# Kernel optimization log

Measured on AMD Instinct MI355X. Metric: run time of the kernel, lower is better.

Reference implementation:

```python
import jax, jax.numpy as jnp
import numpy as np

B, SQ, SK, D = 4, 2048, 2048, 1024


def setup_inputs() -> dict:
    key = jax.random.key(0)
    ks = jax.random.split(key, 8)
    s = 1.0 / np.sqrt(D)
    return {
        "input_seq": jax.random.normal(ks[0], (B, SQ, D), jnp.float32),
        "condition_seq": jax.random.normal(ks[1], (B, SK, D), jnp.float32),
        "Wq": jax.random.normal(ks[2], (D, D), jnp.float32) * s,
        "bq": jnp.zeros((D,), jnp.float32),
        "Wk": jax.random.normal(ks[3], (D, D), jnp.float32) * s,
        "bk": jnp.zeros((D,), jnp.float32),
        "Wv": jax.random.normal(ks[4], (D, D), jnp.float32) * s,
        "bv": jnp.zeros((D,), jnp.float32),
    }


def reference(input_seq, condition_seq, Wq, bq, Wk, bk, Wv, bv):
    # Linear projections (torch Linear: x @ W.T + b)
    q = jnp.einsum("bsd,ed->bse", input_seq, Wq) + bq        # [B,SQ,D]
    k = jnp.einsum("btd,ed->bte", condition_seq, Wk) + bk    # [B,SK,D]
    v = jnp.einsum("btd,ed->bte", condition_seq, Wv) + bv    # [B,SK,D]
    # NOTE: original module omits the 1/sqrt(d) scaling — kept faithful.
    scores = jnp.einsum("bse,bte->bst", q, k)                # [B,SQ,SK]
    attn = jax.nn.softmax(scores, axis=-1)
    attended = jnp.einsum("bst,bte->bse", attn, v)           # [B,SQ,D]
    return attended
```

## Files before the change

### kernel.cpp

```cpp
#include <hip/hip_runtime.h>

using f32x4  = __attribute__((ext_vector_type(4))) float;
using bf16x8 = __attribute__((ext_vector_type(8))) __bf16;
using f16x8  = __attribute__((ext_vector_type(8))) _Float16;
using u16x4  = __attribute__((ext_vector_type(4))) unsigned short;
using u16x8  = __attribute__((ext_vector_type(8))) unsigned short;

constexpr int Bb = 4, SQn = 2048, SKn = 2048, Dd = 1024;

__device__ __forceinline__ unsigned fbitsu(float x){ union{float f;unsigned u;}c; c.f=x; return c.u; }
__device__ __forceinline__ float ubitsf(unsigned u){ union{unsigned u;float f;}c; c.u=u; return c.f; }
__device__ __forceinline__ unsigned short hi_trunc(float x){ return (unsigned short)(fbitsu(x)>>16); }
__device__ __forceinline__ unsigned short hi_rne(float x){ unsigned u=fbitsu(x); return (unsigned short)((u + 0x7FFFu + ((u>>16)&1u))>>16); }
__device__ __forceinline__ float from_hi(unsigned short h){ return ubitsf(((unsigned)h)<<16); }
__device__ __forceinline__ unsigned short h_rne(float x){ _Float16 h = (_Float16)x; return __builtin_bit_cast(unsigned short, h); }
__device__ __forceinline__ float h2f(unsigned short u){ return (float)__builtin_bit_cast(_Float16, u); }

template<int DT> __device__ __forceinline__ unsigned short cvt_rne(float x){ return DT ? h_rne(x) : hi_rne(x); }
template<int DT> __device__ __forceinline__ float cvt_f(unsigned short u){ return DT ? h2f(u) : from_hi(u); }

__device__ __forceinline__ f32x4 mfma_bf16(bf16x8 a, bf16x8 b, f32x4 c){
    return __builtin_amdgcn_mfma_f32_16x16x32_bf16(a, b, c, 0, 0, 0);
}
__device__ __forceinline__ f32x4 mfma_f16(u16x8 a, u16x8 b, f32x4 c){
    return __builtin_amdgcn_mfma_f32_16x16x32_f16(
        __builtin_bit_cast(f16x8, a), __builtin_bit_cast(f16x8, b), c, 0, 0, 0);
}
template<int DT>
__device__ __forceinline__ f32x4 mfma_u16(u16x8 a, u16x8 b, f32x4 c){
    if constexpr (DT) return mfma_f16(a, b, c);
    else return __builtin_amdgcn_mfma_f32_16x16x32_bf16(
        __builtin_bit_cast(bf16x8, a), __builtin_bit_cast(bf16x8, b), c, 0, 0, 0);
}

__device__ __forceinline__ void gload16(const void* g, void* l){
    __builtin_amdgcn_global_load_lds(
        (const __attribute__((address_space(1))) unsigned int*)g,
        (__attribute__((address_space(3))) unsigned int*)l, 16, 0, 0);
}

__device__ __forceinline__ void xcd_swz(int& bx, int& by){
    const int nx = gridDim.x, nwg = nx * gridDim.y;
    int l = by * nx + bx;
    l = (l & 7) * (nwg >> 3) + (l >> 3);
    bx = l % nx; by = l / nx;
}

__global__ __launch_bounds__(256)
void split2(const float* __restrict__ x, const float* __restrict__ c,
            unsigned short* __restrict__ xh, unsigned short* __restrict__ xl,
            unsigned short* __restrict__ ch, unsigned short* __restrict__ cl,
            int n4)
{
    const int stride = gridDim.x * 256;
    for (int i = blockIdx.x * 256 + threadIdx.x; i < 2 * n4; i += stride) {
        const bool second = (i >= n4);
        const int j = second ? i - n4 : i;
        const float* in = second ? c : x;
        unsigned short* hi = second ? ch : xh;
        unsigned short* lo = second ? cl : xl;
        float a[4]; *(float4*)a = *(const float4*)(in + (size_t)j * 4);
        u16x4 h, l;
#pragma unroll
        for (int r = 0; r < 4; ++r) {
            h[r] = h_rne(a[r]);
            l[r] = h_rne(a[r] - h2f(h[r]));
        }
        *(u16x4*)&hi[(size_t)j * 4] = h;
        *(u16x4*)&lo[(size_t)j * 4] = l;
    }
}

__global__ __launch_bounds__(256)
void cvtW(const float* __restrict__ Wq, const float* __restrict__ Wk,
          const float* __restrict__ Wv,
          unsigned short* __restrict__ oq, unsigned short* __restrict__ ok,
          unsigned short* __restrict__ ov, int n4)
{
    const int stride = gridDim.x * 256;
    for (int i = blockIdx.x * 256 + threadIdx.x; i < 3 * n4; i += stride) {
        const float* src; unsigned short* dst; int j = i;
        if (j < n4)          { src = Wq; dst = oq; }
        else if (j < 2*n4)   { src = Wk; dst = ok; j -= n4; }
        else                 { src = Wv; dst = ov; j -= 2*n4; }
        float a[4]; *(float4*)a = *(const float4*)(src + (size_t)j * 4);
        u16x4 h;
#pragma unroll
        for (int r = 0; r < 4; ++r) h[r] = h_rne(a[r]);
        *(u16x4*)&dst[(size_t)j * 4] = h;
    }
}

template<int TERMS, int BM_, int BN_, int BK_, int EPI, int DT>
__global__ __launch_bounds__(256, 2)
void gemm_tile(const unsigned short* __restrict__ Ahg, const unsigned short* __restrict__ Alg,
               const unsigned short* __restrict__ Bhg, const unsigned short* __restrict__ Blg,
               const float* __restrict__ bias,
               void* __restrict__ O0v, void* __restrict__ O1v,
               int M, int N, int K, long aBS, long bBS, long oBS)
{
    constexpr int ROWB = BK_ * 2;
    constexpr int RPC  = 1024 / ROWB;
    constexpr int CA   = BM_ / RPC;
    constexpr int CB   = BN_ / RPC;
    constexpr int AI   = BM_ / 32;
    constexpr int BJ   = BN_ / 32;
    constexpr int KH   = BK_ / 32;
    static_assert(CA % 4 == 0 && CB % 4 == 0, "chunks divisible by 4 waves");

    __shared__ __align__(16) unsigned short Ash[BM_*BK_], Bsh[BN_*BK_];
    __shared__ __align__(16) unsigned short Asl[TERMS>=2?BM_*BK_:8];
    __shared__ __align__(16) unsigned short Bsl[TERMS==3?BN_*BK_:8];

    const int z = blockIdx.z;
    Ahg += (size_t)z * aBS;
    Bhg += (size_t)z * bBS;
    if (TERMS >= 2) Alg += (size_t)z * aBS;
    if (TERMS == 3) Blg += (size_t)z * bBS;

    int bx = blockIdx.x, by = blockIdx.y;
    xcd_swz(bx, by);

    const int tid = threadIdx.x, lane = tid & 63, w = tid >> 6;
    const int wr = (w >> 1) * (BM_/2), wc = (w & 1) * (BN_/2);
    const int lr = lane & 15, lg = lane >> 4;
    const int m0 = by * BM_, n0 = bx * BN_;
    constexpr int rsh = (ROWB == 64) ? 2 : 3;
    const int rowc = lane >> rsh;
    const int colb = (lane & ((1 << rsh) - 1)) << 4;
    const size_t rsBy = (size_t)K * 2;

    f32x4 acc[AI][BJ] = {};

    for (int k0 = 0; k0 < K; k0 += BK_) {
#pragma unroll
        for (int c4 = 0; c4 < CA/4; ++c4) {
            const int c = c4*4 + w;
            const size_t go = (size_t)(m0 + c*RPC + rowc) * rsBy + (size_t)k0*2 + colb;
            gload16((const char*)Ahg + go, (char*)Ash + c*1024);
            if (TERMS >= 2) gload16((const char*)Alg + go, (char*)Asl + c*1024);
        }
#pragma unroll
        for (int c4 = 0; c4 < CB/4; ++c4) {
            const int c = c4*4 + w;
            const size_t go = (size_t)(n0 + c*RPC + rowc) * rsBy + (size_t)k0*2 + colb;
            gload16((const char*)Bhg + go, (char*)Bsh + c*1024);
            if (TERMS == 3) gload16((const char*)Blg + go, (char*)Bsl + c*1024);
        }
        __syncthreads();

#pragma unroll
        for (int kk = 0; kk < KH; ++kk) {
            u16x8 ah[AI], bh[BJ];
#pragma unroll
            for (int i = 0; i < AI; ++i) ah[i] = *(const u16x8*)&Ash[(wr + i*16 + lr)*BK_ + kk*32 + lg*8];
#pragma unroll
            for (int j = 0; j < BJ; ++j) bh[j] = *(const u16x8*)&Bsh[(wc + j*16 + lr)*BK_ + kk*32 + lg*8];
            if (TERMS == 3) {
                u16x8 al[AI], bl[BJ];
#pragma unroll
                for (int i = 0; i < AI; ++i) al[i] = *(const u16x8*)&Asl[(wr + i*16 + lr)*BK_ + kk*32 + lg*8];
#pragma unroll
                for (int j = 0; j < BJ; ++j) bl[j] = *(const u16x8*)&Bsl[(wc + j*16 + lr)*BK_ + kk*32 + lg*8];
#pragma unroll
                for (int i = 0; i < AI; ++i)
#pragma unroll
                    for (int j = 0; j < BJ; ++j) {
                        acc[i][j] = mfma_u16<DT>(ah[i], bh[j], acc[i][j]);
                        acc[i][j] = mfma_u16<DT>(ah[i], bl[j], acc[i][j]);
                        acc[i][j] = mfma_u16<DT>(al[i], bh[j], acc[i][j]);
                    }
            } else if (TERMS == 2) {
                u16x8 al[AI];
#pragma unroll
                for (int i = 0; i < AI; ++i) al[i] = *(const u16x8*)&Asl[(wr + i*16 + lr)*BK_ + kk*32 + lg*8];
#pragma unroll
                for (int i = 0; i < AI; ++i)
#pragma unroll
                    for (int j = 0; j < BJ; ++j) {
                        acc[i][j] = mfma_u16<DT>(ah[i], bh[j], acc[i][j]);
                        acc[i][j] = mfma_u16<DT>(al[i], bh[j], acc[i][j]);
                    }
            } else {
#pragma unroll
                for (int i = 0; i < AI; ++i)
#pragma unroll
                    for (int j = 0; j < BJ; ++j)
                        acc[i][j] = mfma_u16<DT>(ah[i], bh[j], acc[i][j]);
            }
        }
        __syncthreads();
    }

    if (EPI == 0) {
        float* C = (float*)O0v + (size_t)z * oBS;
#pragma unroll
        for (int j = 0; j < BJ; ++j) {
            const int col = n0 + wc + j*16 + lr;
#pragma unroll
            for (int i = 0; i < AI; ++i)
#pragma unroll
                for (int r = 0; r < 4; ++r)
                    C[(size_t)(m0 + wr + i*16 + lg*4 + r) * N + col] = acc[i][j][r];
        }
    } else {
        unsigned short* Chi = (unsigned short*)O0v + (size_t)z * oBS;
        unsigned short* Clo = (unsigned short*)O1v + (size_t)z * oBS;
#pragma unroll
        for (int j = 0; j < BJ; ++j) {
            const int col = n0 + wc + j*16 + lr;
            const float bc = (EPI == 2) ? bias[col] : 0.f;
#pragma unroll
            for (int i = 0; i < AI; ++i)
#pragma unroll
                for (int r = 0; r < 4; ++r) {
                    const size_t idx = (size_t)(m0 + wr + i*16 + lg*4 + r) * N + col;
                    const float v = acc[i][j][r] + bc;
                    const unsigned short h = cvt_rne<DT>(v);
                    Chi[idx] = h;
                    Clo[idx] = cvt_rne<DT>(v - cvt_f<DT>(h));
                }
        }
    }
}

__global__ __launch_bounds__(256, 2)
void gemm_kv(const unsigned short* __restrict__ Ahg, const unsigned short* __restrict__ Alg,
             const unsigned short* __restrict__ Wk16, const unsigned short* __restrict__ Wv16,
             const float* __restrict__ bk, const float* __restrict__ bv,
             unsigned short* __restrict__ Kh, unsigned short* __restrict__ Vt,
             int M, int N, int K)
{
    constexpr int BM_ = 128, BN_ = 128, BK_ = 32;
    __shared__ __align__(16) unsigned short Ash[BM_*BK_], Asl[BM_*BK_];
    __shared__ __align__(16) unsigned short Bks[BN_*BK_], Bvs[BN_*BK_];

    int bx = blockIdx.x, by = blockIdx.y;
    xcd_swz(bx, by);

    const int tid = threadIdx.x, lane = tid & 63, w = tid >> 6;
    const int wr = (w >> 1) * 64, wc = (w & 1) * 64;
    const int lr = lane & 15, lg = lane >> 4;
    const int m0 = by * BM_, n0 = bx * BN_;
    const int rowc = lane >> 2;
    const int colb = (lane & 3) << 4;
    const size_t rsBy = (size_t)K * 2;

    f32x4 acck[4][4] = {}, accv[4][4] = {};

    for (int k0 = 0; k0 < K; k0 += BK_) {
#pragma unroll
        for (int c4 = 0; c4 < 2; ++c4) {
            const int c = c4*4 + w;
            const size_t goA = (size_t)(m0 + c*16 + rowc) * rsBy + (size_t)k0*2 + colb;
            gload16((const char*)Ahg + goA, (char*)Ash + c*1024);
            gload16((const char*)Alg + goA, (char*)Asl + c*1024);
            const size_t goB = (size_t)(n0 + c*16 + rowc) * rsBy + (size_t)k0*2 + colb;
            gload16((const char*)Wk16 + goB, (char*)Bks + c*1024);
            gload16((const char*)Wv16 + goB, (char*)Bvs + c*1024);
        }
        __syncthreads();

        u16x8 ah[4], al[4], bf[4];
#pragma unroll
        for (int i = 0; i < 4; ++i) {
            ah[i] = *(const u16x8*)&Ash[(wr + i*16 + lr)*BK_ + lg*8];
            al[i] = *(const u16x8*)&Asl[(wr + i*16 + lr)*BK_ + lg*8];
        }
#pragma unroll
        for (int j = 0; j < 4; ++j) bf[j] = *(const u16x8*)&Bks[(wc + j*16 + lr)*BK_ + lg*8];
#pragma unroll
        for (int i = 0; i < 4; ++i)
#pragma unroll
            for (int j = 0; j < 4; ++j) {
                acck[i][j] = mfma_f16(ah[i], bf[j], acck[i][j]);
                acck[i][j] = mfma_f16(al[i], bf[j], acck[i][j]);
            }
#pragma unroll
        for (int j = 0; j < 4; ++j) bf[j] = *(const u16x8*)&Bvs[(wc + j*16 + lr)*BK_ + lg*8];
#pragma unroll
        for (int i = 0; i < 4; ++i)
#pragma unroll
            for (int j = 0; j < 4; ++j) {
                accv[i][j] = mfma_f16(ah[i], bf[j], accv[i][j]);
                accv[i][j] = mfma_f16(al[i], bf[j], accv[i][j]);
            }
        __syncthreads();
    }

#pragma unroll
    for (int j = 0; j < 4; ++j) {
        const int col = n0 + wc + j*16 + lr;
        const float bck = bk[col], bcv = bv[col];
#pragma unroll
        for (int i = 0; i < 4; ++i) {
            const int row0 = m0 + wr + i*16 + lg*4;
#pragma unroll
            for (int r = 0; r < 4; ++r)
                Kh[(size_t)(row0 + r)*N + col] = h_rne(acck[i][j][r] + bck);
            const int b = row0 >> 11, t0 = row0 & 2047;
            u16x4 pk;
#pragma unroll
            for (int r = 0; r < 4; ++r) pk[r] = h_rne(accv[i][j][r] + bcv);
            *(u16x4*)&Vt[(((size_t)b*Dd + col) << 11) + t0] = pk;
        }
    }
}

template<int TERMS, int EPI>
__global__ __launch_bounds__(256, 2)
void gemm_proj(const float* __restrict__ A, const float* __restrict__ Bm,
               const float* __restrict__ bias,
               unsigned short* __restrict__ O0, unsigned short* __restrict__ O1,
               int M, int N, int K)
{
    constexpr int BM_ = 128, BN_ = 64, BK_ = 32;
    __shared__ __align__(16) unsigned short Ash[BM_*BK_], Bsh[BN_*BK_];
    __shared__ __align__(16) unsigned short Asl[TERMS==3?BM_*BK_:8], Bsl[TERMS==3?BN_*BK_:8];

    const int tid = threadIdx.x, lane = tid & 63, w = tid >> 6;
    const int wr = (w >> 1) * 64, wc = (w & 1) * 32;
    const int lr = lane & 15, lg = lane >> 4;
    const int m0 = blockIdx.y * BM_, n0 = blockIdx.x * BN_;

    f32x4 acc[4][2] = {};

    for (int k0 = 0; k0 < K; k0 += BK_) {
        float4 av[4], bv[2];
#pragma unroll
        for (int u = 0; u < 4; ++u) {
            const int f = u*256 + tid;
            av[u] = *(const float4*)(A + (size_t)(m0 + (f >> 3))*K + k0 + ((f & 7) << 2));
        }
#pragma unroll
        for (int u = 0; u < 2; ++u) {
            const int f = u*256 + tid;
            bv[u] = *(const float4*)(Bm + (size_t)(n0 + (f >> 3))*K + k0 + ((f & 7) << 2));
        }
        __syncthreads();
#pragma unroll
        for (int u = 0; u < 4; ++u) {
            const int f = u*256 + tid;
            const int row = f >> 3, ko = (f & 7) << 2;
            float a4[4]; *(float4*)a4 = av[u];
            u16x4 ah;
            if (TERMS == 3) {
                u16x4 al;
#pragma unroll
                for (int j = 0; j < 4; ++j) { ah[j] = hi_trunc(a4[j]); al[j] = hi_trunc(a4[j] - from_hi(ah[j])); }
                *(u16x4*)&Asl[row*BK_ + ko] = al;
            } else {
#pragma unroll
                for (int j = 0; j < 4; ++j) ah[j] = hi_rne(a4[j]);
            }
            *(u16x4*)&Ash[row*BK_ + ko] = ah;
        }
#pragma unroll
        for (int u = 0; u < 2; ++u) {
            const int f = u*256 + tid;
            const int row = f >> 3, ko = (f & 7) << 2;
            float b4[4]; *(float4*)b4 = bv[u];
            u16x4 bh;
            if (TERMS == 3) {
                u16x4 bl;
#pragma unroll
                for (int j = 0; j < 4; ++j) { bh[j] = hi_trunc(b4[j]); bl[j] = hi_trunc(b4[j] - from_hi(bh[j])); }
                *(u16x4*)&Bsl[row*BK_ + ko] = bl;
            } else {
#pragma unroll
                for (int j = 0; j < 4; ++j) bh[j] = hi_rne(b4[j]);
            }
            *(u16x4*)&Bsh[row*BK_ + ko] = bh;
        }
        __syncthreads();

        bf16x8 ah[4], bh[2];
#pragma unroll
        for (int i = 0; i < 4; ++i) ah[i] = *(const bf16x8*)&Ash[(wr + i*16 + lr)*BK_ + lg*8];
#pragma unroll
        for (int j = 0; j < 2; ++j) bh[j] = *(const bf16x8*)&Bsh[(wc + j*16 + lr)*BK_ + lg*8];
        if (TERMS == 3) {
            bf16x8 al[4], bl[2];
#pragma unroll
            for (int i = 0; i < 4; ++i) al[i] = *(const bf16x8*)&Asl[(wr + i*16 + lr)*BK_ + lg*8];
#pragma unroll
            for (int j = 0; j < 2; ++j) bl[j] = *(const bf16x8*)&Bsl[(wc + j*16 + lr)*BK_ + lg*8];
#pragma unroll
            for (int i = 0; i < 4; ++i)
#pragma unroll
                for (int j = 0; j < 2; ++j) {
                    acc[i][j] = mfma_bf16(ah[i], bh[j], acc[i][j]);
                    acc[i][j] = mfma_bf16(ah[i], bl[j], acc[i][j]);
                    acc[i][j] = mfma_bf16(al[i], bh[j], acc[i][j]);
                }
        } else {
#pragma unroll
            for (int i = 0; i < 4; ++i)
#pragma unroll
                for (int j = 0; j < 2; ++j)
                    acc[i][j] = mfma_bf16(ah[i], bh[j], acc[i][j]);
        }
        __syncthreads();
    }

#pragma unroll
    for (int j = 0; j < 2; ++j) {
        const int col = n0 + wc + j*16 + lr;
        const float bc = bias[col];
#pragma unroll
        for (int i = 0; i < 4; ++i) {
            if (EPI == 0) {
#pragma unroll
                for (int r = 0; r < 4; ++r) {
                    const int row = m0 + wr + i*16 + lg*4 + r;
                    const float v = acc[i][j][r] + bc;
                    const unsigned short h = h_rne(v);
                    O0[(size_t)row*N + col] = h;
                    O1[(size_t)row*N + col] = h_rne(v - h2f(h));
                }
            } else if (EPI == 2) {
#pragma unroll
                for (int r = 0; r < 4; ++r) {
                    const int row = m0 + wr + i*16 + lg*4 + r;
                    O0[(size_t)row*N + col] = h_rne(acc[i][j][r] + bc);
                }
            } else {
                const int row0 = m0 + wr + i*16 + lg*4;
                const int b = row0 >> 11, t0 = row0 & 2047;
                u16x4 pk;
#pragma unroll
                for (int r = 0; r < 4; ++r) pk[r] = h_rne(acc[i][j][r] + bc);
                *(u16x4*)&O0[(((size_t)b*Dd + col) << 11) + t0] = pk;
            }
        }
    }
}

__global__ __launch_bounds__(256)
void softmax_sp(unsigned short* __restrict__ Shi, const unsigned short* __restrict__ Slo)
{
    const int tid = threadIdx.x;
    unsigned short* ph = Shi + (size_t)blockIdx.x * SKn;
    const unsigned short* pl = Slo + (size_t)blockIdx.x * SKn;
    __shared__ float red[8];

    u16x4 h0 = *(const u16x4*)&ph[tid*4];
    u16x4 h1 = *(const u16x4*)&ph[1024 + tid*4];
    u16x4 l0 = *(const u16x4*)&pl[tid*4];
    u16x4 l1 = *(const u16x4*)&pl[1024 + tid*4];
    float v[8];
#pragma unroll
    for (int r = 0; r < 4; ++r) {
        v[r]   = h2f(h0[r]) + h2f(l0[r]);
        v[4+r] = h2f(h1[r]) + h2f(l1[r]);
    }
    float m = v[0];
#pragma unroll
    for (int r = 1; r < 8; ++r) m = fmaxf(m, v[r]);
#pragma unroll
    for (int o2 = 32; o2 > 0; o2 >>= 1) m = fmaxf(m, __shfl_down(m, o2));
    if ((tid & 63) == 0) red[tid >> 6] = m;
    __syncthreads();
    m = fmaxf(fmaxf(red[0],red[1]), fmaxf(red[2],red[3]));

    float e[8], s = 0.f;
#pragma unroll
    for (int r = 0; r < 8; ++r) { e[r] = __expf(v[r] - m); s += e[r]; }
#pragma unroll
    for (int o2 = 32; o2 > 0; o2 >>= 1) s += __shfl_down(s, o2);
    if ((tid & 63) == 0) red[4 + (tid >> 6)] = s;
    __syncthreads();
    const float inv = 1.f / ((red[4]+red[5])+(red[6]+red[7]));

    u16x4 p0, p1;
#pragma unroll
    for (int r = 0; r < 4; ++r) { p0[r] = h_rne(e[r]*inv); p1[r] = h_rne(e[4+r]*inv); }
    *(u16x4*)&ph[tid*4] = p0;
    *(u16x4*)&ph[1024 + tid*4] = p1;
}

extern "C" void kernel_launch(void* const* d_in, const int* in_sizes, int n_in,
                              void* d_out, int out_size, void* d_ws, size_t ws_size,
                              hipStream_t stream)
{
    const float* x  = (const float*)d_in[0];
    const float* c  = (const float*)d_in[1];
    const float* Wq = (const float*)d_in[2];
    const float* bq = (const float*)d_in[3];
    const float* Wk = (const float*)d_in[4];
    const float* bk = (const float*)d_in[5];
    const float* Wv = (const float*)d_in[6];
    const float* bv = (const float*)d_in[7];
    float* out = (float*)d_out;

    const size_t nQ = (size_t)Bb * SQn * Dd;
    const size_t sE = (size_t)SQn * SKn;
    const size_t nW = (size_t)Dd * Dd;
    unsigned short* Qh = (unsigned short*)d_ws;
    unsigned short* Ql = Qh + nQ;
    unsigned short* Kh = Ql + nQ;
    unsigned short* Kl = Kh + nQ;
    unsigned short* Vt = Kl + nQ;
    unsigned short* Shi = Vt + nQ;
    unsigned short* Slo = Shi + (size_t)Bb * sE;

    unsigned short* Wq16 = Kl;
    unsigned short* Wk16 = Kl + nW;
    unsigned short* Wv16 = Kl + 2*nW;

    unsigned short* xh = Shi;
    unsigned short* xl = Shi + nQ;
    unsigned short* ch = Slo;
    unsigned short* cl = Slo + nQ;

    const size_t needB = (size_t)(Shi - Qh) * 2 + (size_t)Bb * sE * 2 * 2;
    const bool batched = ws_size >= needB;

    const dim3 blk(256);

    if (batched) {
        split2<<<dim3(4096), blk, 0, stream>>>(x, c, xh, xl, ch, cl, (int)(nQ/4));
        cvtW<<<dim3(1024), blk, 0, stream>>>(Wq, Wk, Wv, Wq16, Wk16, Wv16, (int)(nW/4));

        gemm_tile<2,128,128,32,2,1><<<dim3(Dd/128, (Bb*SQn)/128), blk, 0, stream>>>(
            xh, xl, Wq16, nullptr, bq, Qh, Ql, Bb*SQn, Dd, Dd, 0, 0, 0);
        gemm_kv<<<dim3(Dd/128, (Bb*SKn)/128), blk, 0, stream>>>(
            ch, cl, Wk16, Wv16, bk, bv, Kh, Vt, Bb*SKn, Dd, Dd);

        gemm_tile<2,128,128,32,1,1><<<dim3(SKn/128, SQn/128, Bb), blk, 0, stream>>>(
            Qh, Ql, Kh, nullptr, nullptr, Shi, Slo, SQn, SKn, Dd,
            (long)SQn*Dd, (long)SKn*Dd, (long)sE);
        softmax_sp<<<dim3(Bb*SQn), blk, 0, stream>>>(Shi, Slo);
        gemm_tile<1,128,128,32,0,1><<<dim3(Dd/128, SQn/128, Bb), blk, 0, stream>>>(
            Shi, nullptr, Vt, nullptr, nullptr, out, nullptr, SQn, Dd, SKn,
            (long)sE, (long)Dd*SKn, (long)SQn*Dd);
    } else {
        unsigned short* ShiF = Shi;
        unsigned short* SloF = Shi + sE;
        gemm_proj<3,0><<<dim3(Dd/64, (Bb*SQn)/128), blk, 0, stream>>>(x, Wq, bq, Qh, Ql, Bb*SQn, Dd, Dd);
        gemm_proj<3,2><<<dim3(Dd/64, (Bb*SKn)/128), blk, 0, stream>>>(c, Wk, bk, Kh, nullptr, Bb*SKn, Dd, Dd);
        gemm_proj<1,1><<<dim3(Dd/64, (Bb*SKn)/128), blk, 0, stream>>>(c, Wv, bv, Vt, nullptr, Bb*SKn, Dd, Dd);
        for (int b = 0; b < Bb; ++b) {
            const size_t qoff = (size_t)b * SQn * Dd;
            const size_t koff = (size_t)b * SKn * Dd;
            gemm_tile<2,128,64,32,1,1><<<dim3(SKn/64, SQn/128, 1), blk, 0, stream>>>(
                Qh+qoff, Ql+qoff, Kh+koff, nullptr, nullptr, ShiF, SloF, SQn, SKn, Dd, 0, 0, 0);
            softmax_sp<<<dim3(SQn), blk, 0, stream>>>(ShiF, SloF);
            gemm_tile<1,64,64,32,0,1><<<dim3(Dd/64, SQn/64, 1), blk, 0, stream>>>(
                ShiF, nullptr, Vt+(size_t)b*Dd*SKn, nullptr, nullptr, out+qoff, nullptr,
                SQn, Dd, SKn, 0, 0, 0);
        }
    }
}
```

Before: 287.2 us.

## Double-buffer LDS tiles in projection GEMMs to overlap global loads with MFMA

Both the generic GEMM tile kernel and the fused K/V projection kernel now use two LDS buffers. The next K-slice is prefetched with direct-to-LDS loads while MFMAs run on the current one, and a partial vmcnt wait plus raw s_barrier replaces __syncthreads. This targets the load-latency stalls that serialized each K iteration. It doubles LDS use, which may reduce occupancy under launch_bounds(256,2), and it relies on the LPT count matching the exact number of outstanding loads per thread.

```diff
diff --git a/kernel.cpp b/kernel.cpp
--- a/kernel.cpp
+++ b/kernel.cpp
@@ -106,11 +106,12 @@
     constexpr int AI   = BM_ / 32;
     constexpr int BJ   = BN_ / 32;
     constexpr int KH   = BK_ / 32;
+    constexpr int LPT  = (CA/4)*(TERMS>=2?2:1) + (CB/4)*(TERMS==3?2:1);
     static_assert(CA % 4 == 0 && CB % 4 == 0, "chunks divisible by 4 waves");
 
-    __shared__ __align__(16) unsigned short Ash[BM_*BK_], Bsh[BN_*BK_];
-    __shared__ __align__(16) unsigned short Asl[TERMS>=2?BM_*BK_:8];
-    __shared__ __align__(16) unsigned short Bsl[TERMS==3?BN_*BK_:8];
+    __shared__ __align__(16) unsigned short Ash[2][BM_*BK_], Bsh[2][BN_*BK_];
+    __shared__ __align__(16) unsigned short Asl[TERMS>=2?2:1][TERMS>=2?BM_*BK_:8];
+    __shared__ __align__(16) unsigned short Bsl[TERMS==3?2:1][TERMS==3?BN_*BK_:8];
 
     const int z = blockIdx.z;
     Ahg += (size_t)z * aBS;
@@ -130,38 +131,51 @@
     const int colb = (lane & ((1 << rsh) - 1)) << 4;
     const size_t rsBy = (size_t)K * 2;
 
-    f32x4 acc[AI][BJ] = {};
-
-    for (int k0 = 0; k0 < K; k0 += BK_) {
+    auto stage = [&](int k0, int buf){
 #pragma unroll
         for (int c4 = 0; c4 < CA/4; ++c4) {
             const int c = c4*4 + w;
             const size_t go = (size_t)(m0 + c*RPC + rowc) * rsBy + (size_t)k0*2 + colb;
-            gload16((const char*)Ahg + go, (char*)Ash + c*1024);
-            if (TERMS >= 2) gload16((const char*)Alg + go, (char*)Asl + c*1024);
+            gload16((const char*)Ahg + go, (char*)&Ash[buf][0] + c*1024);
+            if (TERMS >= 2) gload16((const char*)Alg + go, (char*)&Asl[buf][0] + c*1024);
         }
 #pragma unroll
         for (int c4 = 0; c4 < CB/4; ++c4) {
             const int c = c4*4 + w;
             const size_t go = (size_t)(n0 + c*RPC + rowc) * rsBy + (size_t)k0*2 + colb;
-            gload16((const char*)Bhg + go, (char*)Bsh + c*1024);
-            if (TERMS == 3) gload16((const char*)Blg + go, (char*)Bsl + c*1024);
-        }
-        __syncthreads();
+            gload16((const char*)Bhg + go, (char*)&Bsh[buf][0] + c*1024);
+            if (TERMS == 3) gload16((const char*)Blg + go, (char*)&Bsl[buf][0] + c*1024);
+        }
+    };
+
+    f32x4 acc[AI][BJ] = {};
+    const int nt = K / BK_;
+
+    stage(0, 0);
+    for (int t = 0; t < nt; ++t) {
+        const int cur = t & 1;
+        if (t + 1 < nt) {
+            stage((t+1)*BK_, cur ^ 1);
+            asm volatile("s_waitcnt vmcnt(%0)" :: "n"(LPT) : "memory");
+        } else {
+            asm volatile("s_waitcnt vmcnt(0)" ::: "memory");
+        }
+        __builtin_amdgcn_sched_barrier(0);
+        __builtin_amdgcn_s_barrier();
 
 #pragma unroll
         for (int kk = 0; kk < KH; ++kk) {
             u16x8 ah[AI], bh[BJ];
 #pragma unroll
-            for (int i = 0; i < AI; ++i) ah[i] = *(const u16x8*)&Ash[(wr + i*16 + lr)*BK_ + kk*32 + lg*8];
-#pragma unroll
-            for (int j = 0; j < BJ; ++j) bh[j] = *(const u16x8*)&Bsh[(wc + j*16 + lr)*BK_ + kk*32 + lg*8];
+            for (int i = 0; i < AI; ++i) ah[i] = *(const u16x8*)&Ash[cur][(wr + i*16 + lr)*BK_ + kk*32 + lg*8];
+#pragma unroll
+            for (int j = 0; j < BJ; ++j) bh[j] = *(const u16x8*)&Bsh[cur][(wc + j*16 + lr)*BK_ + kk*32 + lg*8];
             if (TERMS == 3) {
                 u16x8 al[AI], bl[BJ];
 #pragma unroll
-                for (int i = 0; i < AI; ++i) al[i] = *(const u16x8*)&Asl[(wr + i*16 + lr)*BK_ + kk*32 + lg*8];
-#pragma unroll
-                for (int j = 0; j < BJ; ++j) bl[j] = *(const u16x8*)&Bsl[(wc + j*16 + lr)*BK_ + kk*32 + lg*8];
+                for (int i = 0; i < AI; ++i) al[i] = *(const u16x8*)&Asl[cur][(wr + i*16 + lr)*BK_ + kk*32 + lg*8];
+#pragma unroll
+                for (int j = 0; j < BJ; ++j) bl[j] = *(const u16x8*)&Bsl[cur][(wc + j*16 + lr)*BK_ + kk*32 + lg*8];
 #pragma unroll
                 for (int i = 0; i < AI; ++i)
 #pragma unroll
@@ -173,7 +187,7 @@
             } else if (TERMS == 2) {
                 u16x8 al[AI];
 #pragma unroll
-                for (int i = 0; i < AI; ++i) al[i] = *(const u16x8*)&Asl[(wr + i*16 + lr)*BK_ + kk*32 + lg*8];
+                for (int i = 0; i < AI; ++i) al[i] = *(const u16x8*)&Asl[cur][(wr + i*16 + lr)*BK_ + kk*32 + lg*8];
 #pragma unroll
                 for (int i = 0; i < AI; ++i)
 #pragma unroll
@@ -189,7 +203,7 @@
                         acc[i][j] = mfma_u16<DT>(ah[i], bh[j], acc[i][j]);
             }
         }
-        __syncthreads();
+        __builtin_amdgcn_s_barrier();
     }
 
     if (EPI == 0) {
@@ -232,8 +246,9 @@
              int M, int N, int K)
 {
     constexpr int BM_ = 128, BN_ = 128, BK_ = 32;
-    __shared__ __align__(16) unsigned short Ash[BM_*BK_], Asl[BM_*BK_];
-    __shared__ __align__(16) unsigned short Bks[BN_*BK_], Bvs[BN_*BK_];
+    constexpr int LPT = 8;
+    __shared__ __align__(16) unsigned short Ash[2][BM_*BK_], Asl[2][BM_*BK_];
+    __shared__ __align__(16) unsigned short Bks[2][BN_*BK_], Bvs[2][BN_*BK_];
 
     int bx = blockIdx.x, by = blockIdx.y;
     xcd_swz(bx, by);
@@ -246,29 +261,42 @@
     const int colb = (lane & 3) << 4;
     const size_t rsBy = (size_t)K * 2;
 
-    f32x4 acck[4][4] = {}, accv[4][4] = {};
-
-    for (int k0 = 0; k0 < K; k0 += BK_) {
+    auto stage = [&](int k0, int buf){
 #pragma unroll
         for (int c4 = 0; c4 < 2; ++c4) {
             const int c = c4*4 + w;
             const size_t goA = (size_t)(m0 + c*16 + rowc) * rsBy + (size_t)k0*2 + colb;
-            gload16((const char*)Ahg + goA, (char*)Ash + c*1024);
-            gload16((const char*)Alg + goA, (char*)Asl + c*1024);
+            gload16((const char*)Ahg + goA, (char*)&Ash[buf][0] + c*1024);
+            gload16((const char*)Alg + goA, (char*)&Asl[buf][0] + c*1024);
             const size_t goB = (size_t)(n0 + c*16 + rowc) * rsBy + (size_t)k0*2 + colb;
-            gload16((const char*)Wk16 + goB, (char*)Bks + c*1024);
-            gload16((const char*)Wv16 + goB, (char*)Bvs + c*1024);
-        }
-        __syncthreads();
+            gload16((const char*)Wk16 + goB, (char*)&Bks[buf][0] + c*1024);
+            gload16((const char*)Wv16 + goB, (char*)&Bvs[buf][0] + c*1024);
+        }
+    };
+
+    f32x4 acck[4][4] = {}, accv[4][4] = {};
+    const int nt = K / BK_;
+
+    stage(0, 0);
+    for (int t = 0; t < nt; ++t) {
+        const int cur = t & 1;
+        if (t + 1 < nt) {
+            stage((t+1)*BK_, cur ^ 1);
+            asm volatile("s_waitcnt vmcnt(%0)" :: "n"(LPT) : "memory");
+        } else {
+            asm volatile("s_waitcnt vmcnt(0)" ::: "memory");
+        }
+        __builtin_amdgcn_sched_barrier(0);
+        __builtin_amdgcn_s_barrier();
 
         u16x8 ah[4], al[4], bf[4];
 #pragma unroll
         for (int i = 0; i < 4; ++i) {
-            ah[i] = *(const u16x8*)&Ash[(wr + i*16 + lr)*BK_ + lg*8];
-            al[i] = *(const u16x8*)&Asl[(wr + i*16 + lr)*BK_ + lg*8];
-        }
-#pragma unroll
-        for (int j = 0; j < 4; ++j) bf[j] = *(const u16x8*)&Bks[(wc + j*16 + lr)*BK_ + lg*8];
+            ah[i] = *(const u16x8*)&Ash[cur][(wr + i*16 + lr)*BK_ + lg*8];
+            al[i] = *(const u16x8*)&Asl[cur][(wr + i*16 + lr)*BK_ + lg*8];
+        }
+#pragma unroll
+        for (int j = 0; j < 4; ++j) bf[j] = *(const u16x8*)&Bks[cur][(wc + j*16 + lr)*BK_ + lg*8];
 #pragma unroll
         for (int i = 0; i < 4; ++i)
 #pragma unroll
@@ -277,7 +305,7 @@
                 acck[i][j] = mfma_f16(al[i], bf[j], acck[i][j]);
             }
 #pragma unroll
-        for (int j = 0; j < 4; ++j) bf[j] = *(const u16x8*)&Bvs[(wc + j*16 + lr)*BK_ + lg*8];
+        for (int j = 0; j < 4; ++j) bf[j] = *(const u16x8*)&Bvs[cur][(wc + j*16 + lr)*BK_ + lg*8];
 #pragma unroll
         for (int i = 0; i < 4; ++i)
 #pragma unroll
@@ -285,7 +313,7 @@
                 accv[i][j] = mfma_f16(ah[i], bf[j], accv[i][j]);
                 accv[i][j] = mfma_f16(al[i], bf[j], accv[i][j]);
             }
-        __syncthreads();
+        __builtin_amdgcn_s_barrier();
     }
 
 #pragma unroll
```

Result: slower. 293.1 us (+2.0%).
